# Kernel optimization log

Measured on AMD Instinct MI355X. Metric: run time of the kernel, lower is better.

Reference implementation:

```python
import jax, jax.numpy as jnp
import numpy as np

N_NODES = 16500   # 100 battles x 165 hexes
N_EDGES = 100000  # per link type
K = 3             # number of link types (HeteroConv branches)
C_IN, C_HID, C_OUT = 170, 256, 256
GEN_EPS = 1e-7    # GENConv eps
BN_EPS = 1e-5     # BatchNorm1d eps


def setup_inputs() -> dict:
    key = jax.random.key(0)
    ki = iter(jax.random.split(key, 32))
    inp = {}
    inp["x"] = jax.random.normal(next(ki), (N_NODES, C_IN), jnp.float32)
    inp["edge_index"] = jax.random.randint(next(ki), (K, 2, N_EDGES), 0, N_NODES, dtype=jnp.int32)
    inp["edge_attr"] = jax.random.normal(next(ki), (K, N_EDGES, 1), jnp.float32)

    def uni(k, fan_in, shape):
        b = float(1.0 / np.sqrt(fan_in))
        return jax.random.uniform(k, shape, jnp.float32, -b, b)

    dims = [(C_IN, C_HID), (C_HID, C_HID), (C_HID, C_OUT)]
    for l, (ci, co) in enumerate(dims):
        inp[f"We{l}"] = uni(next(ki), 1, (K, 1, ci))          # edge encoder Linear(1, ci)
        inp[f"be{l}"] = jnp.zeros((K, ci), jnp.float32)
        inp[f"Wa{l}"] = uni(next(ki), ci, (K, ci, 2 * ci))     # MLP layer 1 (expansion=2)
        inp[f"ba{l}"] = jnp.zeros((K, 2 * ci), jnp.float32)
        inp[f"g{l}"] = jnp.ones((K, 2 * ci), jnp.float32)      # BatchNorm gamma
        inp[f"bt{l}"] = jnp.zeros((K, 2 * ci), jnp.float32)    # BatchNorm beta
        inp[f"Wb{l}"] = uni(next(ki), 2 * ci, (K, 2 * ci, co)) # MLP layer 2
        inp[f"bb{l}"] = jnp.zeros((K, co), jnp.float32)
    return inp


def _genconv(x, src, dst, ea, We, be, Wa, ba, g, bt, Wb, bb):
    """PyG GENConv (aggr='softmax', t=1, eps=1e-7, norm='batch') with self loops."""
    n = x.shape[0]
    loops = jnp.arange(n, dtype=src.dtype)
    src = jnp.concatenate([src, loops])
    dst = jnp.concatenate([dst, loops])
    ea = jnp.concatenate([ea, jnp.ones((n, ea.shape[1]), ea.dtype)], axis=0)
    e = ea @ We + be                           # [E+N, ci] edge encoder
    msg = jax.nn.relu(x[src] + e) + GEN_EPS    # [E+N, ci] message
    # per-destination, per-channel segment softmax aggregation
    mx = jax.ops.segment_max(msg, dst, num_segments=n)
    w = jnp.exp(msg - mx[dst])
    den = jax.ops.segment_sum(w, dst, num_segments=n)
    aggr = jax.ops.segment_sum(msg * w, dst, num_segments=n) / den
    out = aggr + x                             # residual with root node
    # MLP: Linear -> BatchNorm(train stats) -> ReLU -> Linear
    h = out @ Wa + ba
    mu = h.mean(axis=0)
    var = ((h - mu) ** 2).mean(axis=0)
    h = (h - mu) * jax.lax.rsqrt(var + BN_EPS) * g + bt
    h = jax.nn.relu(h)
    return h @ Wb + bb


_conv_k = jax.vmap(_genconv, in_axes=(None, 0, 0, 0, 0, 0, 0, 0, 0, 0, 0, 0))


def _forward(x, edge_index, edge_attr, layers):
    h = x
    for i, p in enumerate(layers):
        # HeteroConv: run GENConv per link type, sum-aggregate over types
        h = _conv_k(h, edge_index[:, 0], edge_index[:, 1], edge_attr, *p).sum(axis=0)
        if i < len(layers) - 1:
            h = jax.nn.leaky_relu(h, 0.01)
    return h


def reference(x, edge_index, edge_attr,
              We0, be0, Wa0, ba0, g0, bt0, Wb0, bb0,
              We1, be1, Wa1, ba1, g1, bt1, Wb1, bb1,
              We2, be2, Wa2, ba2, g2, bt2, Wb2, bb2):
    layers = [(We0, be0, Wa0, ba0, g0, bt0, Wb0, bb0),
              (We1, be1, Wa1, ba1, g1, bt1, Wb1, bb1),
              (We2, be2, Wa2, ba2, g2, bt2, Wb2, bb2)]
    return _forward(x, edge_index, edge_attr, layers)
```

## Files before the change

kernel.cpp:

```cpp
#include <hip/hip_runtime.h>
#include <math.h>

#define NN 16500
#define NP 16512
#define NE 100000
#define KT 3

typedef __attribute__((ext_vector_type(8))) short bf8_t;
typedef __attribute__((ext_vector_type(4))) float f4_t;

__device__ __forceinline__ unsigned short f2bf(float f) {
    unsigned int u = __float_as_uint(f);
    u += 0x7fffu + ((u >> 16) & 1u);
    return (unsigned short)(u >> 16);
}
__device__ __forceinline__ float bf2f(unsigned short h) {
    return __uint_as_float(((unsigned int)h) << 16);
}
__device__ __forceinline__ void gload16(unsigned short* lds, const unsigned short* g) {
    __builtin_amdgcn_global_load_lds(
        (const __attribute__((address_space(1))) void*)g,
        (__attribute__((address_space(3))) void*)lds, 16, 0, 0);
}


__global__ void deg_kernel(const int* __restrict__ ei, int* __restrict__ deg) {
    int t = blockIdx.x * blockDim.x + threadIdx.x;
    if (t >= KT * NE) return;
    int k = t / NE, e = t - k * NE;
    int d = ei[k * 2 * NE + NE + e];
    atomicAdd(&deg[k * NN + d], 1);
}

__global__ void scan_kernel(const int* __restrict__ deg, int* __restrict__ offs,
                            int* __restrict__ cursor) {
    int k = blockIdx.x;
    const int* dg = deg + k * NN;
    int* of = offs + k * (NN + 1);
    int* cu = cursor + k * NN;
    __shared__ int part[256];
    int tid = threadIdx.x;
    const int chunk = (NN + 255) / 256;
    int s0 = tid * chunk, s1 = min(NN, s0 + chunk);
    if (s0 > s1) s0 = s1;
    int sum = 0;
    for (int i = s0; i < s1; ++i) sum += dg[i];
    part[tid] = sum;
    __syncthreads();
    for (int off = 1; off < 256; off <<= 1) {
        int v = part[tid];
        int vp = (tid >= off) ? part[tid - off] : 0;
        __syncthreads();
        part[tid] = v + vp;
        __syncthreads();
    }
    int run = (tid == 0) ? 0 : part[tid - 1];
    for (int i = s0; i < s1; ++i) {
        of[i] = run; cu[i] = run;
        run += dg[i];
    }
    if (tid == 255) of[NN] = run;
}

__global__ void scatter_kernel(const int* __restrict__ ei, const float* __restrict__ ea,
                               int* __restrict__ cursor, int2* __restrict__ se) {
    int t = blockIdx.x * blockDim.x + threadIdx.x;
    if (t >= KT * NE) return;
    int k = t / NE, e = t - k * NE;
    int s = ei[k * 2 * NE + e];
    int d = ei[k * 2 * NE + NE + e];
    float a = ea[(size_t)k * NE + e];
    int pos = atomicAdd(&cursor[k * NN + d], 1);
    int2 p; p.x = s; p.y = __float_as_int(a);
    se[(size_t)k * NE + pos] = p;
}


template<int CI, bool BF16X>
__device__ __forceinline__ void loadrow4(float out[4], const void* xv, int s, int c0) {
    if (BF16X) {
        const unsigned short* xb = (const unsigned short*)xv;
        uint2 u = *(const uint2*)(xb + (size_t)s * CI + c0);
        out[0] = bf2f((unsigned short)(u.x & 0xffffu));
        out[1] = bf2f((unsigned short)(u.x >> 16));
        out[2] = bf2f((unsigned short)(u.y & 0xffffu));
        out[3] = bf2f((unsigned short)(u.y >> 16));
    } else {
        const float* p = (const float*)xv + (size_t)s * CI + c0;
        if (c0 + 4 <= CI) {
            float2 ab = *(const float2*)p;
            float2 cd = *(const float2*)(p + 2);
            out[0] = ab.x; out[1] = ab.y; out[2] = cd.x; out[3] = cd.y;
        } else {
            #pragma unroll
            for (int e = 0; e < 4; ++e) out[e] = (c0 + e < CI) ? p[e] : 0.f;
        }
    }
}

template<int CI, bool BF16X>
__global__ __launch_bounds__(256) void aggr_kernel(
    const void* __restrict__ xv, const int2* __restrict__ se_all,
    const int* __restrict__ offs_all,
    const float* __restrict__ We_all, const float* __restrict__ be_all,
    unsigned short* __restrict__ out_hi)
{
    constexpr int KP = (CI + 31) / 32 * 32;
    int k = blockIdx.y;
    int wv = threadIdx.x >> 6, lane = threadIdx.x & 63;
    int c0 = lane * 4;
    unsigned short* o = out_hi + (size_t)k * NP * KP;
    const int2*  se   = se_all + (size_t)k * NE;
    const int*   offs = offs_all + k * (NN + 1);
    const float* We   = We_all + (size_t)k * CI;
    const float* be   = be_all + (size_t)k * CI;

    constexpr bool ACT_ALL = (64 * 4 == KP) && (CI == KP);
    bool act = ACT_ALL || (c0 < CI);
    float w[4], b[4];
    #pragma unroll
    for (int e = 0; e < 4; ++e) {
        bool a = (c0 + e) < CI;
        w[e] = a ? We[c0 + e] : 0.f;
        b[e] = a ? be[c0 + e] : 0.f;
    }

    for (int it = 0; it < 4; ++it) {
        int d = blockIdx.x * 16 + it * 4 + wv;
        if (d >= NN) {
            if (c0 < KP) { uint2 z = {0u, 0u}; *(uint2*)(o + (size_t)d * KP + c0) = z; }
            continue;
        }
        float xd[4] = {0.f, 0.f, 0.f, 0.f};
        if (act) loadrow4<CI, BF16X>(xd, xv, d, c0);
        #pragma unroll
        for (int e = 0; e < 4; ++e) if ((c0 + e) >= CI) xd[e] = 0.f;

        float den[4], num[4];
        #pragma unroll
        for (int e = 0; e < 4; ++e) {
            float mg = fmaxf(xd[e] + w[e] + b[e], 0.f);
            float ex = __expf(mg);
            den[e] = ex;
            num[e] = mg * ex;
        }

        auto step = [&](const float xc[4], float a) {
            #pragma unroll
            for (int e = 0; e < 4; ++e) {
                float t = xc[e] + fmaf(a, w[e], b[e]);
                float mg = fmaxf(t, 0.f);
                float ex = __expf(mg);
                den[e] += ex;
                num[e] = fmaf(mg, ex, num[e]);
            }
        };

        int start = offs[d], end = offs[d + 1];
        for (int base = start; base < end; base += 64) {
            int cnt = min(64, end - base);
            int sv = 0; float av = 0.f;
            if (lane < cnt) {
                int2 p = se[base + lane];
                sv = p.x; av = __int_as_float(p.y);
            }
            float x0[4] = {0.f,0.f,0.f,0.f}, x1[4] = {0.f,0.f,0.f,0.f};
            float x2[4] = {0.f,0.f,0.f,0.f}, x3[4] = {0.f,0.f,0.f,0.f};
            {
                int sA = __shfl(sv, 0), sB = __shfl(sv, 1);
                int sC = __shfl(sv, 2), sD = __shfl(sv, 3);
                if (act)            loadrow4<CI, BF16X>(x0, xv, sA, c0);
                if (act && cnt > 1) loadrow4<CI, BF16X>(x1, xv, sB, c0);
                if (act && cnt > 2) loadrow4<CI, BF16X>(x2, xv, sC, c0);
                if (act && cnt > 3) loadrow4<CI, BF16X>(x3, xv, sD, c0);
            }
            int j = 0;
            for (; j + 3 < cnt; j += 4) {
                float a0 = __shfl(av, j),     a1 = __shfl(av, j + 1);
                float a2 = __shfl(av, j + 2), a3 = __shfl(av, j + 3);
                int s4 = __shfl(sv, (j + 4) & 63), s5 = __shfl(sv, (j + 5) & 63);
                int s6 = __shfl(sv, (j + 6) & 63), s7 = __shfl(sv, (j + 7) & 63);
                step(x0, a0);
                if (act && (j + 4) < cnt) loadrow4<CI, BF16X>(x0, xv, s4, c0);
                step(x1, a1);
                if (act && (j + 5) < cnt) loadrow4<CI, BF16X>(x1, xv, s5, c0);
                step(x2, a2);
                if (act && (j + 6) < cnt) loadrow4<CI, BF16X>(x2, xv, s6, c0);
                step(x3, a3);
                if (act && (j + 7) < cnt) loadrow4<CI, BF16X>(x3, xv, s7, c0);
            }
            if (j < cnt)     step(x0, __shfl(av, j));
            if (j + 1 < cnt) step(x1, __shfl(av, j + 1));
            if (j + 2 < cnt) step(x2, __shfl(av, j + 2));
        }
        if (c0 < KP) {
            unsigned short r[4];
            #pragma unroll
            for (int e = 0; e < 4; ++e) {
                float v = ((c0 + e) < CI) ? (num[e] / den[e] + xd[e]) : 0.f;
                r[e] = f2bf(v);
            }
            uint2 pk = {(unsigned)r[0] | ((unsigned)r[1] << 16),
                        (unsigned)r[2] | ((unsigned)r[3] << 16)};
            *(uint2*)(o + (size_t)d * KP + c0) = pk;
        }
    }
}


struct SplitJob { const float* W; unsigned short* out; int kdim, ndim, np_, kp; };
struct SplitJobs { SplitJob j[6]; };

__global__ void split_all_kernel(SplitJobs jobs) {
    SplitJob jb = jobs.j[blockIdx.z];
    int idx = blockIdx.x * 256 + threadIdx.x;
    int total = KT * jb.np_ * jb.kp;
    if (idx >= total) return;
    int k = idx / (jb.np_ * jb.kp);
    int rem = idx - k * jb.np_ * jb.kp;
    int n = rem / jb.kp;
    int kk = rem - n * jb.kp;
    float v = (n < jb.ndim && kk < jb.kdim) ? jb.W[((size_t)k * jb.kdim + kk) * jb.ndim + n] : 0.f;
    jb.out[idx] = f2bf(v);
}


__global__ __launch_bounds__(256, 3) void gemm1_mfma(
    const unsigned short* __restrict__ A_hi,
    const unsigned short* __restrict__ B_hi,
    const float* __restrict__ bias_all, unsigned short* __restrict__ C_all,
    float* __restrict__ psum,
    int KP, int ldc, int Mv, int Nv)
{
    __shared__ unsigned short Ah[128 * 32];
    __shared__ unsigned short Bh[128 * 32];

    int z = blockIdx.z;
    int gxT = gridDim.x, gyT = gridDim.y;
    int NHP = gxT * 128;
    const unsigned short* Ahg = A_hi + (size_t)z * NP * KP;
    const unsigned short* Bhg = B_hi + (size_t)z * NHP * KP;
    const float* bias = bias_all + (size_t)z * Nv;
    unsigned short* C = C_all + (size_t)z * NP * ldc;

    int tid = threadIdx.x;
    int w = tid >> 6, l = tid & 63;
    int bm = blockIdx.y * 128, bn = blockIdx.x * 128;
    int lane15 = l & 15, quad = l >> 4;
    int wm = (w >> 1) * 64, wn = (w & 1) * 64;
    int srow = l & 15;
    int scol = (l >> 4) * 8;

    f4_t acc[4][4];
    #pragma unroll
    for (int i = 0; i < 4; ++i)
        #pragma unroll
        for (int j = 0; j < 4; ++j) { f4_t zz = {0.f,0.f,0.f,0.f}; acc[i][j] = zz; }

    size_t aoff0 = (size_t)(bm + 32 * w +  0 + srow) * KP + scol;
    size_t aoff1 = (size_t)(bm + 32 * w + 16 + srow) * KP + scol;
    size_t boff0 = (size_t)(bn + 32 * w +  0 + srow) * KP + scol;
    size_t boff1 = (size_t)(bn + 32 * w + 16 + srow) * KP + scol;
    int rb0 = 32 * w, rb1 = 32 * w + 16;
    int ta = (w >> 1) * 4, tb = (w & 1) * 4;

    for (int k0 = 0; k0 < KP; k0 += 32) {
        gload16(&Ah[rb0 * 32], Ahg + aoff0 + k0);
        gload16(&Ah[rb1 * 32], Ahg + aoff1 + k0);
        gload16(&Bh[rb0 * 32], Bhg + boff0 + k0);
        gload16(&Bh[rb1 * 32], Bhg + boff1 + k0);
        __syncthreads();

        bf8_t fa[4], fb[4];
        #pragma unroll
        for (int i = 0; i < 4; ++i) {
            fa[i] = *(const bf8_t*)&Ah[(ta + i) * 512 + l * 8];
            fb[i] = *(const bf8_t*)&Bh[(tb + i) * 512 + l * 8];
        }
        #pragma unroll
        for (int i = 0; i < 4; ++i)
            #pragma unroll
            for (int j = 0; j < 4; ++j)
                acc[i][j] = __builtin_amdgcn_mfma_f32_16x16x32_bf16(fa[i], fb[j], acc[i][j], 0, 0, 0);
        __syncthreads();
    }

    #pragma unroll
    for (int j = 0; j < 4; ++j) {
        int c = bn + wn + j * 16 + lane15;
        float bc = (c < Nv) ? bias[c] : 0.f;
        float s1 = 0.f, s2 = 0.f;
        #pragma unroll
        for (int i = 0; i < 4; ++i) {
            #pragma unroll
            for (int r5 = 0; r5 < 4; ++r5) {
                int r = bm + wm + i * 16 + quad * 4 + r5;
                float v = acc[i][j][r5] + bc;
                unsigned short q = f2bf(v);
                if (r < Mv && c < Nv) C[(size_t)r * ldc + c] = q;
                bool ok = (r < NN) && (c < Nv);
                float vq = ok ? bf2f(q) : 0.f;
                s1 += vq;
                s2 = fmaf(vq, vq, s2);
            }
        }
        s1 += __shfl_xor(s1, 16); s2 += __shfl_xor(s2, 16);
        s1 += __shfl_xor(s1, 32); s2 += __shfl_xor(s2, 32);
        if (quad == 0) {
            int wrow = w >> 1;
            int col = wn + j * 16 + lane15;
            size_t o = ((((size_t)z * gyT + blockIdx.y) * gxT + blockIdx.x) * 2 + wrow) * 256 + col * 2;
            float2 st = {s1, s2};
            *(float2*)&psum[o] = st;
        }
    }
}


__global__ __launch_bounds__(512) void finalize_kernel(
    const float* __restrict__ psum,
    const float* __restrict__ g_all, const float* __restrict__ bt_all,
    float* __restrict__ scale_all, float* __restrict__ shift_all,
    int hid, int gxT)
{
    int z = blockIdx.x;
    int c = threadIdx.x;
    if (c >= hid) return;
    int gx = c >> 7, col = c & 127;
    double s1 = 0.0, s2 = 0.0;
    for (int gy = 0; gy < NP / 128; ++gy) {
        size_t base = (((size_t)z * (NP / 128) + gy) * gxT + gx) * 2 * 256 + col * 2;
        float2 a  = *(const float2*)&psum[base];
        float2 b2 = *(const float2*)&psum[base + 256];
        s1 += (double)a.x + b2.x;
        s2 += (double)a.y + b2.y;
    }
    double mu = s1 / NN;
    double var = s2 / NN - mu * mu;
    if (var < 0.0) var = 0.0;
    float rs = (float)(1.0 / sqrt(var + 1e-5));
    float sc = rs * g_all[(size_t)z * hid + c];
    scale_all[(size_t)z * 512 + c] = sc;
    shift_all[(size_t)z * 512 + c] = bt_all[(size_t)z * hid + c] - (float)mu * sc;
}


__global__ __launch_bounds__(256, 3) void gemm2_mfma(
    const unsigned short* __restrict__ h_all, const float* __restrict__ scale_all,
    const float* __restrict__ shift_all,
    const unsigned short* __restrict__ B_hi,
    float* __restrict__ P_all, int KP, int hid, int Mv)
{
    __shared__ unsigned short Ah[128 * 32];
    __shared__ unsigned short Bh[128 * 32];

    int z = blockIdx.z;
    const unsigned short* hz = h_all + (size_t)z * NP * KP;
    const float* scl = scale_all + (size_t)z * 512;
    const float* shf = shift_all + (size_t)z * 512;
    const unsigned short* Bhg = B_hi + (size_t)z * 256 * KP;
    float* P = P_all + (size_t)z * NP * 256;

    int tid = threadIdx.x;
    int w = tid >> 6, l = tid & 63;
    int bm = blockIdx.y * 128, bn = blockIdx.x * 128;
    int lane15 = l & 15, quad = l >> 4;
    int wm = (w >> 1) * 64, wn = (w & 1) * 64;
    int srow = l & 15, scol = (l >> 4) * 8;

    f4_t acc[4][4];
    #pragma unroll
    for (int i = 0; i < 4; ++i)
        #pragma unroll
        for (int j = 0; j < 4; ++j) { f4_t zz = {0.f,0.f,0.f,0.f}; acc[i][j] = zz; }

    size_t boff0 = (size_t)(bn + 32 * w +  0 + srow) * KP + scol;
    size_t boff1 = (size_t)(bn + 32 * w + 16 + srow) * KP + scol;
    int rb0 = 32 * w, rb1 = 32 * w + 16;
    int ta = (w >> 1) * 4, tb = (w & 1) * 4;

    for (int k0 = 0; k0 < KP; k0 += 32) {
        gload16(&Bh[rb0 * 32], Bhg + boff0 + k0);
        gload16(&Bh[rb1 * 32], Bhg + boff1 + k0);

        #pragma unroll
        for (int sseg = 0; sseg < 2; ++sseg) {
            int L = sseg * 256 + tid;
            int chunk = (L >> 4) & 3;
            int grow = ((L >> 6) << 4) + (L & 15);
            int c = k0 + chunk * 8;
            uint4 hv = *(const uint4*)(hz + (size_t)(bm + grow) * KP + c);
            float4 s0 = *(const float4*)(scl + c);
            float4 s1 = *(const float4*)(scl + c + 4);
            float4 t0 = *(const float4*)(shf + c);
            float4 t1 = *(const float4*)(shf + c + 4);
            unsigned int uu[4] = {hv.x, hv.y, hv.z, hv.w};
            float ss[8] = {s0.x, s0.y, s0.z, s0.w, s1.x, s1.y, s1.z, s1.w};
            float tt[8] = {t0.x, t0.y, t0.z, t0.w, t1.x, t1.y, t1.z, t1.w};
            bf8_t hi8;
            #pragma unroll
            for (int e = 0; e < 8; ++e) {
                unsigned short hb = (e & 1) ? (unsigned short)(uu[e >> 1] >> 16)
                                            : (unsigned short)(uu[e >> 1] & 0xffffu);
                float x = bf2f(hb);
                float val = (c + e < hid) ? fmaxf(fmaf(x, ss[e], tt[e]), 0.f) : 0.f;
                hi8[e] = (short)f2bf(val);
            }
            *(bf8_t*)&Ah[L * 8] = hi8;
        }
        __syncthreads();

        bf8_t fa[4], fb[4];
        #pragma unroll
        for (int i = 0; i < 4; ++i) {
            fa[i] = *(const bf8_t*)&Ah[(ta + i) * 512 + l * 8];
            fb[i] = *(const bf8_t*)&Bh[(tb + i) * 512 + l * 8];
        }
        #pragma unroll
        for (int i = 0; i < 4; ++i)
            #pragma unroll
            for (int j = 0; j < 4; ++j)
                acc[i][j] = __builtin_amdgcn_mfma_f32_16x16x32_bf16(fa[i], fb[j], acc[i][j], 0, 0, 0);
        __syncthreads();
    }

    #pragma unroll
    for (int i = 0; i < 4; ++i)
        #pragma unroll
        for (int j = 0; j < 4; ++j) {
            int c = bn + wn + j * 16 + lane15;
            #pragma unroll
            for (int r5 = 0; r5 < 4; ++r5) {
                int r = bm + wm + i * 16 + quad * 4 + r5;
                if (r < Mv)
                    P[(size_t)r * 256 + c] = acc[i][j][r5];
            }
        }
}


__global__ __launch_bounds__(256) void reduce_kernel(
    const float* __restrict__ P, const float* __restrict__ bb,
    float* __restrict__ outf, unsigned short* __restrict__ outb,
    int leaky, int as_bf16)
{
    int idx = blockIdx.x * 256 + threadIdx.x;
    if (idx >= NN * 64) return;
    int r = idx >> 6, c = (idx & 63) * 4;
    const float4 p0 = *(const float4*)&P[((size_t)0 * NP + r) * 256 + c];
    const float4 p1 = *(const float4*)&P[((size_t)1 * NP + r) * 256 + c];
    const float4 p2 = *(const float4*)&P[((size_t)2 * NP + r) * 256 + c];
    const float4 b0 = *(const float4*)&bb[c];
    const float4 b1 = *(const float4*)&bb[256 + c];
    const float4 b2 = *(const float4*)&bb[512 + c];
    float v[4] = {p0.x + p1.x + p2.x + b0.x + b1.x + b2.x,
                  p0.y + p1.y + p2.y + b0.y + b1.y + b2.y,
                  p0.z + p1.z + p2.z + b0.z + b1.z + b2.z,
                  p0.w + p1.w + p2.w + b0.w + b1.w + b2.w};
    if (leaky) {
        #pragma unroll
        for (int e = 0; e < 4; ++e) v[e] = (v[e] > 0.f) ? v[e] : 0.01f * v[e];
    }
    if (as_bf16) {
        unsigned int o0 = (unsigned int)f2bf(v[0]) | ((unsigned int)f2bf(v[1]) << 16);
        unsigned int o1 = (unsigned int)f2bf(v[2]) | ((unsigned int)f2bf(v[3]) << 16);
        uint2 o = {o0, o1};
        *(uint2*)&outb[(size_t)r * 256 + c] = o;
    } else {
        float4 o = {v[0], v[1], v[2], v[3]};
        *(float4*)&outf[(size_t)r * 256 + c] = o;
    }
}


extern "C" void kernel_launch(void* const* d_in, const int* in_sizes, int n_in,
                              void* d_out, int out_size, void* d_ws, size_t ws_size,
                              hipStream_t stream)
{
    const float* x  = (const float*)d_in[0];
    const int*   ei = (const int*)d_in[1];
    const float* ea = (const float*)d_in[2];

    char* w = (char*)d_ws;
    auto alloc = [&](size_t bytes) {
        char* p = w;
        w += (bytes + 255) & ~(size_t)255;
        return p;
    };
    int* deg    = (int*)alloc((size_t)KT * NN * 4);
    int* offs   = (int*)alloc((size_t)KT * (NN + 1) * 4);
    int* cursor = (int*)alloc((size_t)KT * NN * 4);
    int2* se    = (int2*)alloc((size_t)KT * NE * 8);
    unsigned short* a1_hi = (unsigned short*)alloc((size_t)KT * NP * 256 * 2);
    unsigned short* h3 = (unsigned short*)alloc((size_t)KT * NP * 512 * 2);
    float* partial = (float*)alloc((size_t)KT * NP * 256 * 4);
    unsigned short* bta_l[3];
    unsigned short* btb_l[3];
    for (int l = 0; l < 3; ++l) {
        bta_l[l] = (unsigned short*)alloc((size_t)KT * 512 * 256 * 2);
        btb_l[l] = (unsigned short*)alloc((size_t)KT * 256 * 512 * 2);
    }
    float* psum = (float*)alloc((size_t)KT * (NP / 128) * 4 * 2 * 256 * 4);
    float* scale3 = (float*)alloc((size_t)KT * 512 * 4);
    float* shift3 = (float*)alloc((size_t)KT * 512 * 4);
    unsigned short* bufA = (unsigned short*)alloc((size_t)NN * 256 * 2);
    unsigned short* bufB = (unsigned short*)alloc((size_t)NN * 256 * 2);

    hipMemsetAsync(deg, 0, (size_t)KT * NN * 4, stream);
    int net = KT * NE;
    deg_kernel<<<(net + 255) / 256, 256, 0, stream>>>(ei, deg);
    scan_kernel<<<KT, 256, 0, stream>>>(deg, offs, cursor);
    scatter_kernel<<<(net + 255) / 256, 256, 0, stream>>>(ei, ea, cursor, se);

    SplitJobs jobs;
    int maxtot = 0;
    for (int l = 0; l < 3; ++l) {
        int ci  = (l == 0) ? 170 : 256;
        int KP1 = (ci + 31) / 32 * 32;
        int hid = 2 * ci;
        int NHP = (hid + 127) / 128 * 128;
        int KP2 = (hid + 31) / 32 * 32;
        jobs.j[2 * l]     = { (const float*)d_in[3 + 8 * l + 2], bta_l[l], ci,  hid, NHP, KP1 };
        jobs.j[2 * l + 1] = { (const float*)d_in[3 + 8 * l + 6], btb_l[l], hid, 256, 512, KP2 };
        maxtot = max(maxtot, KT * NHP * KP1);
        maxtot = max(maxtot, KT * 256 * KP2);
    }
    for (int l = 0; l < 3; ++l) {
        int ci  = (l == 0) ? 170 : 256;
        int hid = 2 * ci;
        int KP2 = (hid + 31) / 32 * 32;
        jobs.j[2 * l + 1].np_ = 256;
        maxtot = max(maxtot, KT * 256 * KP2);
    }
    dim3 gsp((maxtot + 255) / 256, 1, 6);
    split_all_kernel<<<gsp, 256, 0, stream>>>(jobs);

    const void* hin = x;
    for (int l = 0; l < 3; ++l) {
        int ci  = (l == 0) ? 170 : 256;
        int KP1 = (ci + 31) / 32 * 32;
        int hid = 2 * ci;
        int NHP = (hid + 127) / 128 * 128;
        int KP2 = (hid + 31) / 32 * 32;
        const float* We = (const float*)d_in[3 + 8 * l + 0];
        const float* be = (const float*)d_in[3 + 8 * l + 1];
        const float* ba = (const float*)d_in[3 + 8 * l + 3];
        const float* g  = (const float*)d_in[3 + 8 * l + 4];
        const float* bt = (const float*)d_in[3 + 8 * l + 5];
        const float* bb = (const float*)d_in[3 + 8 * l + 7];

        dim3 ga(NP / 16, KT);
        if (l == 0)
            aggr_kernel<170, false><<<ga, 256, 0, stream>>>(hin, se, offs, We, be, a1_hi);
        else
            aggr_kernel<256, true><<<ga, 256, 0, stream>>>(hin, se, offs, We, be, a1_hi);

        dim3 g1(NHP / 128, NP / 128, KT);
        gemm1_mfma<<<g1, 256, 0, stream>>>(a1_hi, bta_l[l], ba, h3, psum, KP1, KP2, NN, hid);

        finalize_kernel<<<KT, 512, 0, stream>>>(psum, g, bt, scale3, shift3, hid, NHP / 128);

        dim3 g2(2, NP / 128, KT);
        gemm2_mfma<<<g2, 256, 0, stream>>>(h3, scale3, shift3, btb_l[l],
                                           partial, KP2, hid, NP);

        unsigned short* outb = (l == 0) ? bufA : bufB;
        reduce_kernel<<<(NN * 64 + 255) / 256, 256, 0, stream>>>(
            partial, bb, (float*)d_out, outb, (l < 2) ? 1 : 0, (l < 2) ? 1 : 0);

        hin = (l < 2) ? (const void*)outb : nullptr;
    }
}
```

Before: 674.0 us.

## Fuse type-sum into second GEMM, double-buffer GEMM tiles, parallelize BN finalize

The second MLP GEMM now accumulates over all three link types inside one kernel, treating them as a concatenated K dimension. Bias, leaky ReLU and the bf16 store are applied in its epilogue, which removes the fp32 partial buffer and the separate reduce kernel. Both GEMMs get double-buffered LDS tiles so the next K-slice load overlaps the MFMAs on the current one. The BN finalize now uses more blocks with a shared-memory partial reduction. The trade-off is that gemm2 switches to 64-row tiles with a serial 3x longer K loop and lower occupancy (launch bounds 2).

```diff
diff --git a/kernel.cpp b/kernel.cpp
--- a/kernel.cpp
+++ b/kernel.cpp
@@ -232,8 +232,8 @@
     float* __restrict__ psum,
     int KP, int ldc, int Mv, int Nv)
 {
-    __shared__ unsigned short Ah[128 * 32];
-    __shared__ unsigned short Bh[128 * 32];
+    __shared__ unsigned short Ah[2][128 * 32];
+    __shared__ unsigned short Bh[2][128 * 32];
 
     int z = blockIdx.z;
     int gxT = gridDim.x, gyT = gridDim.y;
@@ -264,18 +264,25 @@
     int rb0 = 32 * w, rb1 = 32 * w + 16;
     int ta = (w >> 1) * 4, tb = (w & 1) * 4;
 
-    for (int k0 = 0; k0 < KP; k0 += 32) {
-        gload16(&Ah[rb0 * 32], Ahg + aoff0 + k0);
-        gload16(&Ah[rb1 * 32], Ahg + aoff1 + k0);
-        gload16(&Bh[rb0 * 32], Bhg + boff0 + k0);
-        gload16(&Bh[rb1 * 32], Bhg + boff1 + k0);
-        __syncthreads();
+    gload16(&Ah[0][rb0 * 32], Ahg + aoff0);
+    gload16(&Ah[0][rb1 * 32], Ahg + aoff1);
+    gload16(&Bh[0][rb0 * 32], Bhg + boff0);
+    gload16(&Bh[0][rb1 * 32], Bhg + boff1);
+    __syncthreads();
+
+    int cur = 0;
+    for (int k0 = 32; k0 < KP; k0 += 32) {
+        int nxt = cur ^ 1;
+        gload16(&Ah[nxt][rb0 * 32], Ahg + aoff0 + k0);
+        gload16(&Ah[nxt][rb1 * 32], Ahg + aoff1 + k0);
+        gload16(&Bh[nxt][rb0 * 32], Bhg + boff0 + k0);
+        gload16(&Bh[nxt][rb1 * 32], Bhg + boff1 + k0);
 
         bf8_t fa[4], fb[4];
         #pragma unroll
         for (int i = 0; i < 4; ++i) {
-            fa[i] = *(const bf8_t*)&Ah[(ta + i) * 512 + l * 8];
-            fb[i] = *(const bf8_t*)&Bh[(tb + i) * 512 + l * 8];
+            fa[i] = *(const bf8_t*)&Ah[cur][(ta + i) * 512 + l * 8];
+            fb[i] = *(const bf8_t*)&Bh[cur][(tb + i) * 512 + l * 8];
         }
         #pragma unroll
         for (int i = 0; i < 4; ++i)
@@ -283,6 +290,20 @@
             for (int j = 0; j < 4; ++j)
                 acc[i][j] = __builtin_amdgcn_mfma_f32_16x16x32_bf16(fa[i], fb[j], acc[i][j], 0, 0, 0);
         __syncthreads();
+        cur = nxt;
+    }
+    {
+        bf8_t fa[4], fb[4];
+        #pragma unroll
+        for (int i = 0; i < 4; ++i) {
+            fa[i] = *(const bf8_t*)&Ah[cur][(ta + i) * 512 + l * 8];
+            fb[i] = *(const bf8_t*)&Bh[cur][(tb + i) * 512 + l * 8];
+        }
+        #pragma unroll
+        for (int i = 0; i < 4; ++i)
+            #pragma unroll
+            for (int j = 0; j < 4; ++j)
+                acc[i][j] = __builtin_amdgcn_mfma_f32_16x16x32_bf16(fa[i], fb[j], acc[i][j], 0, 0, 0);
     }
 
     #pragma unroll
@@ -317,158 +338,166 @@
 }
 
 
-__global__ __launch_bounds__(512) void finalize_kernel(
+__global__ __launch_bounds__(256) void finalize_kernel(
     const float* __restrict__ psum,
     const float* __restrict__ g_all, const float* __restrict__ bt_all,
     float* __restrict__ scale_all, float* __restrict__ shift_all,
     int hid, int gxT)
 {
     int z = blockIdx.x;
-    int c = threadIdx.x;
-    if (c >= hid) return;
-    int gx = c >> 7, col = c & 127;
+    int t64 = threadIdx.x & 63;
+    int slice = threadIdx.x >> 6;
+    int c = blockIdx.y * 64 + t64;
+    __shared__ double rs1[4][64];
+    __shared__ double rs2[4][64];
     double s1 = 0.0, s2 = 0.0;
-    for (int gy = 0; gy < NP / 128; ++gy) {
-        size_t base = (((size_t)z * (NP / 128) + gy) * gxT + gx) * 2 * 256 + col * 2;
-        float2 a  = *(const float2*)&psum[base];
-        float2 b2 = *(const float2*)&psum[base + 256];
-        s1 += (double)a.x + b2.x;
-        s2 += (double)a.y + b2.y;
-    }
-    double mu = s1 / NN;
-    double var = s2 / NN - mu * mu;
-    if (var < 0.0) var = 0.0;
-    float rs = (float)(1.0 / sqrt(var + 1e-5));
-    float sc = rs * g_all[(size_t)z * hid + c];
-    scale_all[(size_t)z * 512 + c] = sc;
-    shift_all[(size_t)z * 512 + c] = bt_all[(size_t)z * hid + c] - (float)mu * sc;
-}
-
-
-__global__ __launch_bounds__(256, 3) void gemm2_mfma(
+    if (c < gxT * 128) {
+        int gx = c >> 7, col = c & 127;
+        for (int gy = slice; gy < NP / 128; gy += 4) {
+            size_t base = (((size_t)z * (NP / 128) + gy) * gxT + gx) * 2 * 256 + col * 2;
+            float2 a  = *(const float2*)&psum[base];
+            float2 b2 = *(const float2*)&psum[base + 256];
+            s1 += (double)a.x + b2.x;
+            s2 += (double)a.y + b2.y;
+        }
+    }
+    rs1[slice][t64] = s1;
+    rs2[slice][t64] = s2;
+    __syncthreads();
+    if (slice == 0 && c < hid) {
+        double S1 = rs1[0][t64] + rs1[1][t64] + rs1[2][t64] + rs1[3][t64];
+        double S2 = rs2[0][t64] + rs2[1][t64] + rs2[2][t64] + rs2[3][t64];
+        double mu = S1 / NN;
+        double var = S2 / NN - mu * mu;
+        if (var < 0.0) var = 0.0;
+        float rs = (float)(1.0 / sqrt(var + 1e-5));
+        float sc = rs * g_all[(size_t)z * hid + c];
+        scale_all[(size_t)z * 512 + c] = sc;
+        shift_all[(size_t)z * 512 + c] = bt_all[(size_t)z * hid + c] - (float)mu * sc;
+    }
+}
+
+
+__device__ __forceinline__ bf8_t bnpack(uint4 hv, float4 s0, float4 s1,
+                                        float4 t0, float4 t1, int ch0, int hid) {
+    unsigned int uu[4] = {hv.x, hv.y, hv.z, hv.w};
+    float ss[8] = {s0.x, s0.y, s0.z, s0.w, s1.x, s1.y, s1.z, s1.w};
+    float tt[8] = {t0.x, t0.y, t0.z, t0.w, t1.x, t1.y, t1.z, t1.w};
+    bf8_t r;
+    #pragma unroll
+    for (int e = 0; e < 8; ++e) {
+        unsigned short hb = (e & 1) ? (unsigned short)(uu[e >> 1] >> 16)
+                                    : (unsigned short)(uu[e >> 1] & 0xffffu);
+        float x = bf2f(hb);
+        float val = (ch0 + e < hid) ? fmaxf(fmaf(x, ss[e], tt[e]), 0.f) : 0.f;
+        r[e] = (short)f2bf(val);
+    }
+    return r;
+}
+
+__global__ __launch_bounds__(256, 2) void gemm2_mfma(
     const unsigned short* __restrict__ h_all, const float* __restrict__ scale_all,
     const float* __restrict__ shift_all,
     const unsigned short* __restrict__ B_hi,
-    float* __restrict__ P_all, int KP, int hid, int Mv)
+    const float* __restrict__ bb,
+    float* __restrict__ outf, unsigned short* __restrict__ outb,
+    int KP, int hid, int leaky, int as_bf16)
 {
-    __shared__ unsigned short Ah[128 * 32];
-    __shared__ unsigned short Bh[128 * 32];
-
-    int z = blockIdx.z;
-    const unsigned short* hz = h_all + (size_t)z * NP * KP;
-    const float* scl = scale_all + (size_t)z * 512;
-    const float* shf = shift_all + (size_t)z * 512;
-    const unsigned short* Bhg = B_hi + (size_t)z * 256 * KP;
-    float* P = P_all + (size_t)z * NP * 256;
+    __shared__ unsigned short Ah[2][64 * 32];
+    __shared__ unsigned short Bh[2][128 * 32];
 
     int tid = threadIdx.x;
     int w = tid >> 6, l = tid & 63;
-    int bm = blockIdx.y * 128, bn = blockIdx.x * 128;
+    int bm = blockIdx.y * 64, bn = blockIdx.x * 128;
     int lane15 = l & 15, quad = l >> 4;
-    int wm = (w >> 1) * 64, wn = (w & 1) * 64;
+    int wm = (w >> 1) * 32, wn = (w & 1) * 64;
     int srow = l & 15, scol = (l >> 4) * 8;
 
-    f4_t acc[4][4];
+    const int KPZ = KP / 32;
+    const int NIT = 3 * KPZ;
+
+    f4_t acc[2][4];
     #pragma unroll
-    for (int i = 0; i < 4; ++i)
+    for (int i = 0; i < 2; ++i)
         #pragma unroll
         for (int j = 0; j < 4; ++j) { f4_t zz = {0.f,0.f,0.f,0.f}; acc[i][j] = zz; }
 
-    size_t boff0 = (size_t)(bn + 32 * w +  0 + srow) * KP + scol;
-    size_t boff1 = (size_t)(bn + 32 * w + 16 + srow) * KP + scol;
     int rb0 = 32 * w, rb1 = 32 * w + 16;
-    int ta = (w >> 1) * 4, tb = (w & 1) * 4;
-
-    for (int k0 = 0; k0 < KP; k0 += 32) {
-        gload16(&Bh[rb0 * 32], Bhg + boff0 + k0);
-        gload16(&Bh[rb1 * 32], Bhg + boff1 + k0);
-
-        #pragma unroll
-        for (int sseg = 0; sseg < 2; ++sseg) {
-            int L = sseg * 256 + tid;
-            int chunk = (L >> 4) & 3;
-            int grow = ((L >> 6) << 4) + (L & 15);
-            int c = k0 + chunk * 8;
-            uint4 hv = *(const uint4*)(hz + (size_t)(bm + grow) * KP + c);
-            float4 s0 = *(const float4*)(scl + c);
-            float4 s1 = *(const float4*)(scl + c + 4);
-            float4 t0 = *(const float4*)(shf + c);
-            float4 t1 = *(const float4*)(shf + c + 4);
-            unsigned int uu[4] = {hv.x, hv.y, hv.z, hv.w};
-            float ss[8] = {s0.x, s0.y, s0.z, s0.w, s1.x, s1.y, s1.z, s1.w};
-            float tt[8] = {t0.x, t0.y, t0.z, t0.w, t1.x, t1.y, t1.z, t1.w};
-            bf8_t hi8;
-            #pragma unroll
-            for (int e = 0; e < 8; ++e) {
-                unsigned short hb = (e & 1) ? (unsigned short)(uu[e >> 1] >> 16)
-                                            : (unsigned short)(uu[e >> 1] & 0xffffu);
-                float x = bf2f(hb);
-                float val = (c + e < hid) ? fmaxf(fmaf(x, ss[e], tt[e]), 0.f) : 0.f;
-                hi8[e] = (short)f2bf(val);
-            }
-            *(bf8_t*)&Ah[L * 8] = hi8;
-        }
-        __syncthreads();
-
-        bf8_t fa[4], fb[4];
-        #pragma unroll
-        for (int i = 0; i < 4; ++i) {
-            fa[i] = *(const bf8_t*)&Ah[(ta + i) * 512 + l * 8];
-            fb[i] = *(const bf8_t*)&Bh[(tb + i) * 512 + l * 8];
-        }
-        #pragma unroll
-        for (int i = 0; i < 4; ++i)
+    int ta = (w >> 1) * 2, tb = (w & 1) * 4;
+    int grow = ((tid >> 6) << 4) + (tid & 15);
+    int ccol = ((tid >> 4) & 3) * 8;
+
+    size_t arow = (size_t)(bm + grow) * KP + ccol;
+    size_t brow0 = (size_t)(bn + 32 * w + srow) * KP + scol;
+    size_t brow1 = (size_t)(bn + 32 * w + 16 + srow) * KP + scol;
+
+    {
+        uint4 hv = *(const uint4*)(h_all + arow);
+        gload16(&Bh[0][rb0 * 32], B_hi + brow0);
+        gload16(&Bh[0][rb1 * 32], B_hi + brow1);
+        const float* scl = scale_all + ccol;
+        const float* shf = shift_all + ccol;
+        float4 s0 = *(const float4*)scl, s1 = *(const float4*)(scl + 4);
+        float4 t0 = *(const float4*)shf, t1 = *(const float4*)(shf + 4);
+        *(bf8_t*)&Ah[0][tid * 8] = bnpack(hv, s0, s1, t0, t1, ccol, hid);
+    }
+    __syncthreads();
+
+    int cur = 0;
+    for (int it = 0; it < NIT; ++it) {
+        int nit = it + 1;
+        bool have = nit < NIT;
+        int nxt = cur ^ 1;
+        uint4 hv;
+        float4 s0, s1, t0, t1;
+        int nch = 0;
+        if (have) {
+            int nzz = nit / KPZ, nkk = (nit - nzz * KPZ) * 32;
+            nch = nkk + ccol;
+            hv = *(const uint4*)(h_all + (size_t)nzz * NP * KP + arow + nkk);
+            const float* scl = scale_all + (size_t)nzz * 512 + nch;
+            const float* shf = shift_all + (size_t)nzz * 512 + nch;
+            s0 = *(const float4*)scl; s1 = *(const float4*)(scl + 4);
+            t0 = *(const float4*)shf; t1 = *(const float4*)(shf + 4);
+            const unsigned short* bz = B_hi + (size_t)nzz * 256 * KP + nkk;
+            gload16(&Bh[nxt][rb0 * 32], bz + brow0);
+            gload16(&Bh[nxt][rb1 * 32], bz + brow1);
+        }
+        bf8_t fa[2], fb[4];
+        #pragma unroll
+        for (int i = 0; i < 2; ++i)
+            fa[i] = *(const bf8_t*)&Ah[cur][(ta + i) * 512 + l * 8];
+        #pragma unroll
+        for (int j = 0; j < 4; ++j)
+            fb[j] = *(const bf8_t*)&Bh[cur][(tb + j) * 512 + l * 8];
+        #pragma unroll
+        for (int i = 0; i < 2; ++i)
             #pragma unroll
             for (int j = 0; j < 4; ++j)
                 acc[i][j] = __builtin_amdgcn_mfma_f32_16x16x32_bf16(fa[i], fb[j], acc[i][j], 0, 0, 0);
+        if (have)
+            *(bf8_t*)&Ah[nxt][tid * 8] = bnpack(hv, s0, s1, t0, t1, nch, hid);
         __syncthreads();
+        cur = nxt;
     }
 
     #pragma unroll
-    for (int i = 0; i < 4; ++i)
-        #pragma unroll
-        for (int j = 0; j < 4; ++j) {
-            int c = bn + wn + j * 16 + lane15;
+    for (int j = 0; j < 4; ++j) {
+        int c = bn + wn + j * 16 + lane15;
+        float bsum = bb[c] + bb[256 + c] + bb[512 + c];
+        #pragma unroll
+        for (int i = 0; i < 2; ++i) {
             #pragma unroll
             for (int r5 = 0; r5 < 4; ++r5) {
                 int r = bm + wm + i * 16 + quad * 4 + r5;
-                if (r < Mv)
-                    P[(size_t)r * 256 + c] = acc[i][j][r5];
-            }
-        }
-}
-
-
-__global__ __launch_bounds__(256) void reduce_kernel(
-    const float* __restrict__ P, const float* __restrict__ bb,
-    float* __restrict__ outf, unsigned short* __restrict__ outb,
-    int leaky, int as_bf16)
-{
-    int idx = blockIdx.x * 256 + threadIdx.x;
-    if (idx >= NN * 64) return;
-    int r = idx >> 6, c = (idx & 63) * 4;
-    const float4 p0 = *(const float4*)&P[((size_t)0 * NP + r) * 256 + c];
-    const float4 p1 = *(const float4*)&P[((size_t)1 * NP + r) * 256 + c];
-    const float4 p2 = *(const float4*)&P[((size_t)2 * NP + r) * 256 + c];
-    const float4 b0 = *(const float4*)&bb[c];
-    const float4 b1 = *(const float4*)&bb[256 + c];
-    const float4 b2 = *(const float4*)&bb[512 + c];
-    float v[4] = {p0.x + p1.x + p2.x + b0.x + b1.x + b2.x,
-                  p0.y + p1.y + p2.y + b0.y + b1.y + b2.y,
-                  p0.z + p1.z + p2.z + b0.z + b1.z + b2.z,
-                  p0.w + p1.w + p2.w + b0.w + b1.w + b2.w};
-    if (leaky) {
-        #pragma unroll
-        for (int e = 0; e < 4; ++e) v[e] = (v[e] > 0.f) ? v[e] : 0.01f * v[e];
-    }
-    if (as_bf16) {
-        unsigned int o0 = (unsigned int)f2bf(v[0]) | ((unsigned int)f2bf(v[1]) << 16);
-        unsigned int o1 = (unsigned int)f2bf(v[2]) | ((unsigned int)f2bf(v[3]) << 16);
-        uint2 o = {o0, o1};
-        *(uint2*)&outb[(size_t)r * 256 + c] = o;
-    } else {
-        float4 o = {v[0], v[1], v[2], v[3]};
-        *(float4*)&outf[(size_t)r * 256 + c] = o;
+                if (r < NN) {
+                    float v = acc[i][j][r5] + bsum;
+                    if (leaky) v = (v > 0.f) ? v : 0.01f * v;
+                    if (as_bf16) outb[(size_t)r * 256 + c] = f2bf(v);
+                    else         outf[(size_t)r * 256 + c] = v;
+                }
+            }
+        }
     }
 }
 
@@ -493,7 +522,6 @@
     int2* se    = (int2*)alloc((size_t)KT * NE * 8);
     unsigned short* a1_hi = (unsigned short*)alloc((size_t)KT * NP * 256 * 2);
     unsigned short* h3 = (unsigned short*)alloc((size_t)KT * NP * 512 * 2);
-    float* partial = (float*)alloc((size_t)KT * NP * 256 * 4);
     unsigned short* bta_l[3];
     unsigned short* btb_l[3];
     for (int l = 0; l < 3; ++l) {
@@ -521,15 +549,8 @@
         int NHP = (hid + 127) / 128 * 128;
         int KP2 = (hid + 31) / 32 * 32;
         jobs.j[2 * l]     = { (const float*)d_in[3 + 8 * l + 2], bta_l[l], ci,  hid, NHP, KP1 };
-        jobs.j[2 * l + 1] = { (const float*)d_in[3 + 8 * l + 6], btb_l[l], hid, 256, 512, KP2 };
+        jobs.j[2 * l + 1] = { (const float*)d_in[3 + 8 * l + 6], btb_l[l], hid, 256, 256, KP2 };
         maxtot = max(maxtot, KT * NHP * KP1);
-        maxtot = max(maxtot, KT * 256 * KP2);
-    }
-    for (int l = 0; l < 3; ++l) {
-        int ci  = (l == 0) ? 170 : 256;
-        int hid = 2 * ci;
-        int KP2 = (hid + 31) / 32 * 32;
-        jobs.j[2 * l + 1].np_ = 256;
         maxtot = max(maxtot, KT * 256 * KP2);
     }
     dim3 gsp((maxtot + 255) / 256, 1, 6);
@@ -558,15 +579,14 @@
         dim3 g1(NHP / 128, NP / 128, KT);
         gemm1_mfma<<<g1, 256, 0, stream>>>(a1_hi, bta_l[l], ba, h3, psum, KP1, KP2, NN, hid);
 
-        finalize_kernel<<<KT, 512, 0, stream>>>(psum, g, bt, scale3, shift3, hid, NHP / 128);
-
-        dim3 g2(2, NP / 128, KT);
-        gemm2_mfma<<<g2, 256, 0, stream>>>(h3, scale3, shift3, btb_l[l],
-                                           partial, KP2, hid, NP);
+        dim3 gf(KT, 8);
+        finalize_kernel<<<gf, 256, 0, stream>>>(psum, g, bt, scale3, shift3, hid, NHP / 128);
 
         unsigned short* outb = (l == 0) ? bufA : bufB;
-        reduce_kernel<<<(NN * 64 + 255) / 256, 256, 0, stream>>>(
-            partial, bb, (float*)d_out, outb, (l < 2) ? 1 : 0, (l < 2) ? 1 : 0);
+        dim3 g2(2, NP / 64);
+        gemm2_mfma<<<g2, 256, 0, stream>>>(h3, scale3, shift3, btb_l[l], bb,
+                                           (float*)d_out, outb, KP2, hid,
+                                           (l < 2) ? 1 : 0, (l < 2) ? 1 : 0);
 
         hin = (l < 2) ? (const void*)outb : nullptr;
     }
```

Result: no change. 671.2 us (-0.4%).
